# Kernel tuning notes

Measured on AMD Instinct MI355X. Metric: run time of the kernel, lower is better.

Reference implementation:

```python
import jax, jax.numpy as jnp
import numpy as np

N = 4_000_000
H, W = 1080, 1920


def setup_inputs() -> dict:
    key = jax.random.key(0)
    ks = jax.random.split(key, 4)
    # points mostly in front of the camera (viewmat = identity)
    means = jax.random.normal(ks[0], (N, 3), jnp.float32) * jnp.array([2.0, 2.0, 1.5], jnp.float32) + jnp.array([0.0, 0.0, 5.0], jnp.float32)
    colors = jax.random.normal(ks[1], (N, 3), jnp.float32)          # pre-sigmoid logits
    opacities = jax.random.normal(ks[2], (N, 1), jnp.float32)       # pre-sigmoid logits (unused by solid rasterizer)
    scales = jax.random.normal(ks[3], (N, 3), jnp.float32) * 0.1 - 5.0
    quats = jnp.concatenate([jnp.ones((N, 1), jnp.float32), jnp.zeros((N, 3), jnp.float32)], axis=1)
    viewmat = jnp.eye(4, dtype=jnp.float32)
    K = jnp.array([[1000.0, 0.0, W / 2.0], [0.0, 1000.0, H / 2.0], [0.0, 0.0, 1.0]], jnp.float32)
    return dict(means=means, colors=colors, opacities=opacities, scales=scales,
                quats=quats, viewmat=viewmat, K=K, height=H, width=W)


def _rasterize_solid(means, colors, viewmat, K, height, width):
    # camera transform
    R = viewmat[:3, :3]
    t = viewmat[:3, 3]
    mc = means @ R.T + t                     # [N,3] points in camera frame
    z = mc[:, 2]
    front = z > 0.1
    z_safe = jnp.where(front, z, 1.0)        # avoid div-by-~0 for culled points
    fx, fy, cx, cy = K[0, 0], K[1, 1], K[0, 2], K[1, 2]
    x = mc[:, 0] * fx / z_safe + cx
    y = mc[:, 1] * fy / z_safe + cy
    on = front & (x >= 0) & (x < width - 1) & (y >= 0) & (y < height - 1)

    x0f = jnp.floor(x)
    y0f = jnp.floor(y)
    dx = x - x0f
    dy = y - y0f
    x0 = jnp.clip(x0f.astype(jnp.int32), 0, width - 1)
    y0 = jnp.clip(y0f.astype(jnp.int32), 0, height - 1)
    x1 = jnp.clip(x0 + 1, 0, width - 1)
    y1 = jnp.clip(y0 + 1, 0, height - 1)
    pix = y0 * width + x0

    # scatter-min reproduces that order-independently. Off points contribute +inf.
    zbuf = jnp.full((height * width,), jnp.inf, means.dtype).at[pix].min(jnp.where(on, z, jnp.inf))
    zbuf = jax.lax.stop_gradient(zbuf)       # only feeds a boolean test, no grad path in torch either
    vis = on & (z <= zbuf[pix] + 0.05)
    visf = vis.astype(means.dtype)

    # bilinear weights; (wb <-> y1x0, wc <-> y0x1) pairing kept faithful to source
    wa = (1 - dx) * (1 - dy) * visf
    wb = dx * (1 - dy) * visf
    wc = (1 - dx) * dy * visf
    wd = dx * dy * visf

    feat = jnp.concatenate([colors, z[:, None]], axis=1)   # [N,4] rgb+depth
    buf = jnp.zeros((height * width, 5), means.dtype)
    for idx, w in ((pix, wa), (y1 * width + x0, wb), (y0 * width + x1, wc), (y1 * width + x1, wd)):
        buf = buf.at[idx].add(jnp.concatenate([feat * w[:, None], w[:, None]], axis=1))

    total = buf[:, 4:5] + 1e-6
    ff = buf[:, 0:4] / total
    rgb = jnp.clip(ff[:, 0:3], 0.0, 1.0)
    return jnp.concatenate([rgb, ff[:, 3:4]], axis=1).reshape(height, width, 4)


def reference(means, colors, opacities, scales, quats, viewmat, K, height, width):
    render_colors = jax.nn.sigmoid(colors)
    _ = jax.nn.sigmoid(opacities)  # computed in torch forward, unused by solid rasterizer
    return _rasterize_solid(means, render_colors, viewmat, K, height, width)
```

## Files before the change

### kernel.cpp

```cpp
#include <hip/hip_runtime.h>
#include <math.h>

#define IMG_H 1080
#define IMG_W 1920
#define NPIX (IMG_H * IMG_W)

#define TILE_W 64
#define TILE_H 8
#define NTX (IMG_W / TILE_W)
#define NTY (IMG_H / TILE_H)
#define NTILES (NTX * NTY)
#define TPIX (TILE_W * TILE_H)

#define NSEG 512
#define SEGT 1024

#define ZMW (TILE_W + 1)
#define ZMH (TILE_H + 1)
#define NBIN (ZMW * ZMH)

#define CAPT 4096
#define CAP 2048

__device__ __attribute__((noinline)) float4 project4(
    const float* __restrict__ vm, const float* __restrict__ Km,
    float mx, float my, float mz)
{
    float mcx = vm[0] * mx + vm[1] * my + vm[2]  * mz + vm[3];
    float mcy = vm[4] * mx + vm[5] * my + vm[6]  * mz + vm[7];
    float mcz = vm[8] * mx + vm[9] * my + vm[10] * mz + vm[11];
    float z = mcz;
    bool front = z > 0.1f;
    float z_safe = front ? z : 1.0f;
    float x = mcx * Km[0] / z_safe + Km[2];
    float y = mcy * Km[4] / z_safe + Km[5];
    return make_float4(x, y, z, front ? 1.0f : 0.0f);
}

__device__ __forceinline__ bool on_test(const float4& p)
{
    return (p.w != 0.0f) && (p.x >= 0.0f) && (p.x < (float)(IMG_W - 1))
                         && (p.y >= 0.0f) && (p.y < (float)(IMG_H - 1));
}

__device__ __forceinline__ void project_pt(
    const float* __restrict__ vm, const float* __restrict__ Km,
    float mx, float my, float mz,
    float& x, float& y, float& z, bool& on)
{
    float mcx = vm[0] * mx + vm[1] * my + vm[2]  * mz + vm[3];
    float mcy = vm[4] * mx + vm[5] * my + vm[6]  * mz + vm[7];
    float mcz = vm[8] * mx + vm[9] * my + vm[10] * mz + vm[11];
    z = mcz;
    bool front = z > 0.1f;
    float z_safe = front ? z : 1.0f;
    x = mcx * Km[0] / z_safe + Km[2];
    y = mcy * Km[4] / z_safe + Km[5];
    on = front && (x >= 0.0f) && (x < (float)(IMG_W - 1))
               && (y >= 0.0f) && (y < (float)(IMG_H - 1));
}

__global__ __launch_bounds__(SEGT) void k_count(
    const float* __restrict__ means, const float* __restrict__ vm,
    const float* __restrict__ Km, unsigned int* __restrict__ hist,
    int N, int C)
{
    __shared__ unsigned int h[NTILES];
    int tid = threadIdx.x, w = blockIdx.x;
    for (int t = tid; t < NTILES; t += SEGT) h[t] = 0u;
    __syncthreads();
    int start = w * C, end = min(start + C, N);
    for (int j = start + tid; j < end; j += SEGT) {
        float4 p = project4(vm, Km, means[3 * j], means[3 * j + 1], means[3 * j + 2]);
        if (!on_test(p)) continue;
        int x0 = (int)floorf(p.x), y0 = (int)floorf(p.y);
        int tx0 = x0 >> 6, ty0 = y0 >> 3;
        int tx1 = (x0 + 1) >> 6, ty1 = (y0 + 1) >> 3;
#pragma unroll
        for (int sy = 0; sy < 2; ++sy) {
            int ty = sy ? ty1 : ty0;
            if (sy && ty1 == ty0) continue;
#pragma unroll
            for (int sx = 0; sx < 2; ++sx) {
                int tx = sx ? tx1 : tx0;
                if (sx && tx1 == tx0) continue;
                atomicAdd(&h[ty * NTX + tx], 1u);
            }
        }
    }
    __syncthreads();
    for (int t = tid; t < NTILES; t += SEGT)
        hist[(size_t)w * NTILES + t] = h[t];
}

__global__ __launch_bounds__(256) void k_colpref(
    const unsigned int* __restrict__ hist, unsigned int* __restrict__ histBase,
    unsigned int* __restrict__ tileBase)
{
    int t = blockIdx.x * 256 + threadIdx.x;
    if (t >= NTILES) return;
    unsigned int run = 0u;
#pragma unroll 8
    for (int w = 0; w < NSEG; ++w) {
        unsigned int v = hist[(size_t)w * NTILES + t];
        histBase[(size_t)w * NTILES + t] = run;
        run += v;
    }
    tileBase[t] = run;
}

__global__ __launch_bounds__(256) void k_scan(unsigned int* __restrict__ tileBase)
{
    __shared__ unsigned int part[256];
    int tid = threadIdx.x;
    unsigned int loc[16];
    unsigned int sum = 0u;
#pragma unroll
    for (int i = 0; i < 16; ++i) {
        int t = tid * 16 + i;
        unsigned int v = (t < NTILES) ? tileBase[t] : 0u;
        loc[i] = sum;
        sum += v;
    }
    part[tid] = sum;
    __syncthreads();
    if (tid == 0) {
        unsigned int run = 0u;
        for (int i = 0; i < 256; ++i) {
            unsigned int v = part[i];
            part[i] = run;
            run += v;
        }
        tileBase[NTILES] = run;
    }
    __syncthreads();
    unsigned int base = part[tid];
#pragma unroll
    for (int i = 0; i < 16; ++i) {
        int t = tid * 16 + i;
        if (t < NTILES) tileBase[t] = base + loc[i];
    }
}

__global__ __launch_bounds__(SEGT) void k_binscatter(
    const float* __restrict__ means, const float* __restrict__ colors,
    const float* __restrict__ vm, const float* __restrict__ Km,
    const unsigned int* __restrict__ histBase,
    const unsigned int* __restrict__ tileBase,
    float4* __restrict__ records, int N, int C, unsigned int cap)
{
    __shared__ unsigned int cur[NTILES];
    int tid = threadIdx.x, w = blockIdx.x;
    for (int t = tid; t < NTILES; t += SEGT)
        cur[t] = tileBase[t] + histBase[(size_t)w * NTILES + t];
    __syncthreads();
    int start = w * C, end = min(start + C, N);
    for (int j = start + tid; j < end; j += SEGT) {
        float4 p = project4(vm, Km, means[3 * j], means[3 * j + 1], means[3 * j + 2]);
        if (!on_test(p)) continue;
        float r = 1.0f / (1.0f + expf(-colors[3 * j]));
        float g = 1.0f / (1.0f + expf(-colors[3 * j + 1]));
        float b = 1.0f / (1.0f + expf(-colors[3 * j + 2]));
        unsigned int ri = (unsigned int)(r * 1023.0f + 0.5f);
        unsigned int gi = (unsigned int)(g * 1023.0f + 0.5f);
        unsigned int bi = (unsigned int)(b * 1023.0f + 0.5f);
        float4 rec = make_float4(p.x, p.y, p.z,
                                 __uint_as_float(ri | (gi << 10) | (bi << 20)));
        int x0 = (int)floorf(p.x), y0 = (int)floorf(p.y);
        int tx0 = x0 >> 6, ty0 = y0 >> 3;
        int tx1 = (x0 + 1) >> 6, ty1 = (y0 + 1) >> 3;
#pragma unroll
        for (int sy = 0; sy < 2; ++sy) {
            int ty = sy ? ty1 : ty0;
            if (sy && ty1 == ty0) continue;
#pragma unroll
            for (int sx = 0; sx < 2; ++sx) {
                int tx = sx ? tx1 : tx0;
                if (sx && tx1 == tx0) continue;
                int t = ty * NTX + tx;
                unsigned int slot = atomicAdd(&cur[t], 1u);
                if (slot < cap) records[slot] = rec;
            }
        }
    }
}

__global__ __launch_bounds__(256) void k_tile_sort(
    const unsigned int* __restrict__ tileBase,
    const float4* __restrict__ records, float* __restrict__ out,
    unsigned int cap)
{
    __shared__ unsigned short sIdx[CAPT];
    __shared__ int sStart[NBIN + 1];
    __shared__ int sCur[NBIN];
    __shared__ float sZmin[NBIN];
    __shared__ int sScan[256];

    int tid = threadIdx.x;
    int t = blockIdx.x;
    int txb = (t % NTX) * TILE_W;
    int tyb = (t / NTX) * TILE_H;

    unsigned int base = tileBase[t], next = tileBase[t + 1];
    int cnt = 0;
    if (base < cap) cnt = (int)min(min(next - base, cap - base), (unsigned int)CAPT);
    const float4* rec = records + base;

    for (int b = tid; b < NBIN; b += 256) sCur[b] = 0;
    __syncthreads();

    int hb[16];
#pragma unroll
    for (int u = 0; u < 16; ++u) {
        int j = tid + u * 256;
        hb[u] = -1;
        if (j < cnt) {
            float4 v = rec[j];
            int x0l = (int)floorf(v.x) - txb;
            int y0l = (int)floorf(v.y) - tyb;
            int b = (y0l + 1) * ZMW + (x0l + 1);
            hb[u] = b;
            atomicAdd(&sCur[b], 1);
        }
    }
    __syncthreads();

    int b0 = tid * 3;
    int c0 = (b0     < NBIN) ? sCur[b0]     : 0;
    int c1 = (b0 + 1 < NBIN) ? sCur[b0 + 1] : 0;
    int c2 = (b0 + 2 < NBIN) ? sCur[b0 + 2] : 0;
    int local = c0 + c1 + c2;
    sScan[tid] = local;
    __syncthreads();
    for (int off = 1; off < 256; off <<= 1) {
        int v = (tid >= off) ? sScan[tid - off] : 0;
        __syncthreads();
        sScan[tid] += v;
        __syncthreads();
    }
    int run = sScan[tid] - local;
    if (b0 < NBIN)     { sStart[b0]     = run;           sCur[b0]     = run; }
    if (b0 + 1 < NBIN) { sStart[b0 + 1] = run + c0;      sCur[b0 + 1] = run + c0; }
    if (b0 + 2 < NBIN) { sStart[b0 + 2] = run + c0 + c1; sCur[b0 + 2] = run + c0 + c1; }
    if (tid == 255) sStart[NBIN] = cnt;
    __syncthreads();

#pragma unroll
    for (int u = 0; u < 16; ++u) {
        if (hb[u] >= 0) {
            int j = tid + u * 256;
            int slot = atomicAdd(&sCur[hb[u]], 1);
            sIdx[slot] = (unsigned short)j;
        }
    }
    __syncthreads();

    for (int b = tid; b < NBIN; b += 256) {
        float zm = 1e30f;
        int e = sStart[b + 1];
        for (int k = sStart[b]; k < e; ++k)
            zm = fminf(zm, rec[sIdx[k]].z);
        sZmin[b] = zm;
    }
    __syncthreads();

    for (int p = tid; p < TPIX; p += 256) {
        int px = p % TILE_W, py = p / TILE_W;
        float ra = 0.0f, ga = 0.0f, ba = 0.0f, za = 0.0f, wsum = 0.0f;
#pragma unroll
        for (int c = 0; c < 4; ++c) {
            int ox = c & 1, oy = c >> 1;
            int hx = px - ox, hy = py - oy;
            int b = (hy + 1) * ZMW + (hx + 1);
            float zlim = sZmin[b] + 0.05f;
            int e = sStart[b + 1];
            for (int k = sStart[b]; k < e; ++k) {
                float4 v = rec[sIdx[k]];
                if (!(v.z <= zlim)) continue;
                float dx = v.x - floorf(v.x);
                float dy = v.y - floorf(v.y);
                float wgt = (oy ? dx : (1.0f - dx)) * (ox ? dy : (1.0f - dy));
                unsigned int rgb = __float_as_uint(v.w);
                ra += (float)(rgb & 1023u) * wgt;
                ga += (float)((rgb >> 10) & 1023u) * wgt;
                ba += (float)((rgb >> 20) & 1023u) * wgt;
                za += v.z * wgt;
                wsum += wgt;
            }
        }
        float tot = wsum + 1e-6f;
        float inv = (1.0f / 1023.0f) / tot;
        float r = ra * inv, g = ga * inv, b2 = ba * inv;
        float zz = za / tot;
        r  = fminf(fmaxf(r, 0.0f), 1.0f);
        g  = fminf(fmaxf(g, 0.0f), 1.0f);
        b2 = fminf(fmaxf(b2, 0.0f), 1.0f);
        int gy = tyb + py, gx = txb + px;
        reinterpret_cast<float4*>(out)[gy * IMG_W + gx] = make_float4(r, g, b2, zz);
    }
}


__global__ __launch_bounds__(256) void k_zmin(
    const float* __restrict__ means, const float* __restrict__ vm,
    const float* __restrict__ Km, unsigned int* __restrict__ zbuf, int N)
{
    int i = blockIdx.x * 256 + threadIdx.x;
    if (i >= N) return;
    float x, y, z; bool on;
    project_pt(vm, Km, means[3 * i], means[3 * i + 1], means[3 * i + 2], x, y, z, on);
    if (!on) return;
    int x0 = (int)floorf(x), y0 = (int)floorf(y);
    atomicMin(&zbuf[y0 * IMG_W + x0], __float_as_uint(z));
}

__global__ __launch_bounds__(256) void k_scatter_u32(
    const float* __restrict__ means, const float* __restrict__ vm,
    const float* __restrict__ Km, const unsigned int* __restrict__ zbuf,
    unsigned int* __restrict__ cursors, unsigned int* __restrict__ records, int N)
{
    int i = blockIdx.x * 256 + threadIdx.x;
    if (i >= N) return;
    float x, y, z; bool on;
    project_pt(vm, Km, means[3 * i], means[3 * i + 1], means[3 * i + 2], x, y, z, on);
    if (!on) return;
    int x0 = (int)floorf(x), y0 = (int)floorf(y);
    int pix = y0 * IMG_W + x0;
    if (!(z <= __uint_as_float(zbuf[pix]) + 0.05f)) return;
    int tx0 = x0 / TILE_W, ty0 = y0 / TILE_H;
    int tx1 = (x0 + 1) / TILE_W, ty1 = (y0 + 1) / TILE_H;
#pragma unroll
    for (int sy = 0; sy < 2; ++sy) {
        int ty = sy ? ty1 : ty0;
        if (sy && ty1 == ty0) continue;
#pragma unroll
        for (int sx = 0; sx < 2; ++sx) {
            int tx = sx ? tx1 : tx0;
            if (sx && tx1 == tx0) continue;
            int t = ty * NTX + tx;
            unsigned int slot = atomicAdd(&cursors[t], 1u);
            if (slot < CAP) records[(size_t)t * CAP + slot] = (unsigned int)i;
        }
    }
}

__global__ __launch_bounds__(256) void k_tile_u32(
    const float* __restrict__ means, const float* __restrict__ colors,
    const float* __restrict__ vm, const float* __restrict__ Km,
    const unsigned int* __restrict__ cursors,
    const unsigned int* __restrict__ records,
    float* __restrict__ out)
{
    __shared__ float sR[TPIX], sG[TPIX], sB[TPIX], sZ[TPIX], sW[TPIX];
    int tid = threadIdx.x;
    int t = blockIdx.x;
    int txb = (t % NTX) * TILE_W;
    int tyb = (t / NTX) * TILE_H;
    for (int p = tid; p < TPIX; p += 256) {
        sR[p] = 0.0f; sG[p] = 0.0f; sB[p] = 0.0f; sZ[p] = 0.0f; sW[p] = 0.0f;
    }
    __syncthreads();

    int cnt = (int)min(cursors[t], (unsigned int)CAP);
    const unsigned int* rec = records + (size_t)t * CAP;
    for (int j = tid; j < cnt; j += 256) {
        int i = (int)rec[j];
        float x, y, z; bool on;
        project_pt(vm, Km, means[3 * i], means[3 * i + 1], means[3 * i + 2], x, y, z, on);
        float x0f = floorf(x), y0f = floorf(y);
        int x0 = (int)x0f, y0 = (int)y0f;
        float dx = x - x0f, dy = y - y0f;
        float wa = (1.0f - dx) * (1.0f - dy);
        float wb = dx * (1.0f - dy);
        float wc = (1.0f - dx) * dy;
        float wd = dx * dy;
        float r = 1.0f / (1.0f + expf(-colors[3 * i]));
        float g = 1.0f / (1.0f + expf(-colors[3 * i + 1]));
        float b = 1.0f / (1.0f + expf(-colors[3 * i + 2]));
        int cxs[4] = { x0, x0, x0 + 1, x0 + 1 };
        int cys[4] = { y0, y0 + 1, y0, y0 + 1 };
        float ws[4] = { wa, wb, wc, wd };
#pragma unroll
        for (int c = 0; c < 4; ++c) {
            int lx = cxs[c] - txb, ly = cys[c] - tyb;
            if ((unsigned)lx < TILE_W && (unsigned)ly < TILE_H) {
                int lp = ly * TILE_W + lx;
                float w = ws[c];
                atomicAdd(&sR[lp], r * w);
                atomicAdd(&sG[lp], g * w);
                atomicAdd(&sB[lp], b * w);
                atomicAdd(&sZ[lp], z * w);
                atomicAdd(&sW[lp], w);
            }
        }
    }
    __syncthreads();

    for (int p = tid; p < TPIX; p += 256) {
        float tot = sW[p] + 1e-6f;
        float r = sR[p] / tot, g = sG[p] / tot, b = sB[p] / tot, zz = sZ[p] / tot;
        r = fminf(fmaxf(r, 0.0f), 1.0f);
        g = fminf(fmaxf(g, 0.0f), 1.0f);
        b = fminf(fmaxf(b, 0.0f), 1.0f);
        int gy = tyb + p / TILE_W, gx = txb + p % TILE_W;
        reinterpret_cast<float4*>(out)[gy * IMG_W + gx] = make_float4(r, g, b, zz);
    }
}


__global__ __launch_bounds__(256) void k_splat(
    const float* __restrict__ means, const float* __restrict__ colors,
    const float* __restrict__ vm, const float* __restrict__ Km,
    const float* __restrict__ zbuf,
    float* __restrict__ acc, float* __restrict__ wsum, int N)
{
    int i = blockIdx.x * 256 + threadIdx.x;
    if (i >= N) return;
    float x, y, z; bool on;
    project_pt(vm, Km, means[3 * i], means[3 * i + 1], means[3 * i + 2], x, y, z, on);
    if (!on) return;
    float x0f = floorf(x), y0f = floorf(y);
    int x0 = (int)x0f, y0 = (int)y0f;
    int pix = y0 * IMG_W + x0;
    if (!(z <= zbuf[pix] + 0.05f)) return;
    float dx = x - x0f, dy = y - y0f;
    float wa = (1.0f - dx) * (1.0f - dy);
    float wb = dx * (1.0f - dy);
    float wc = (1.0f - dx) * dy;
    float wd = dx * dy;
    float r = 1.0f / (1.0f + expf(-colors[3 * i]));
    float g = 1.0f / (1.0f + expf(-colors[3 * i + 1]));
    float b = 1.0f / (1.0f + expf(-colors[3 * i + 2]));
    int ia = pix, ib = pix + IMG_W, ic = pix + 1, id = pix + IMG_W + 1;
#define SPLAT1(idx, w)                                    \
    do {                                                  \
        atomicAdd(&acc[4 * (idx) + 0], r * (w));          \
        atomicAdd(&acc[4 * (idx) + 1], g * (w));          \
        atomicAdd(&acc[4 * (idx) + 2], b * (w));          \
        atomicAdd(&acc[4 * (idx) + 3], z * (w));          \
        atomicAdd(&wsum[(idx)], (w));                     \
    } while (0)
    SPLAT1(ia, wa); SPLAT1(ib, wb); SPLAT1(ic, wc); SPLAT1(id, wd);
#undef SPLAT1
}

__global__ __launch_bounds__(256) void k_final(
    float* __restrict__ out, const float* __restrict__ wsum)
{
    int p = blockIdx.x * 256 + threadIdx.x;
    if (p >= NPIX) return;
    float tot = wsum[p] + 1e-6f;
    float4 v = reinterpret_cast<float4*>(out)[p];
    float r = v.x / tot, g = v.y / tot, b = v.z / tot, zz = v.w / tot;
    r = fminf(fmaxf(r, 0.0f), 1.0f);
    g = fminf(fmaxf(g, 0.0f), 1.0f);
    b = fminf(fmaxf(b, 0.0f), 1.0f);
    reinterpret_cast<float4*>(out)[p] = make_float4(r, g, b, zz);
}

extern "C" void kernel_launch(void* const* d_in, const int* in_sizes, int n_in,
                              void* d_out, int out_size, void* d_ws, size_t ws_size,
                              hipStream_t stream)
{
    const float* means  = (const float*)d_in[0];
    const float* colors = (const float*)d_in[1];
    const float* vm     = (const float*)d_in[5];
    const float* Km     = (const float*)d_in[6];
    int N = in_sizes[0] / 3;
    float* out = (float*)d_out;

    const size_t histB   = (size_t)NSEG * NTILES * 4;
    const size_t tbB     = (size_t)(NTILES + 1) * 4;
    size_t fixedA        = 2 * histB + tbB;
    fixedA               = (fixedA + 15) & ~(size_t)15;
    const size_t zbufB   = (size_t)NPIX * 4;
    const size_t curB    = (size_t)NTILES * 4;
    const size_t recU32B = (size_t)NTILES * CAP * 4;

    if (ws_size >= fixedA + ((size_t)128 << 20)) {
        unsigned int* hist     = (unsigned int*)d_ws;
        unsigned int* histBase = (unsigned int*)((char*)d_ws + histB);
        unsigned int* tileBase = (unsigned int*)((char*)d_ws + 2 * histB);
        float4*       records  = (float4*)((char*)d_ws + fixedA);
        unsigned int  cap      = (unsigned int)min((ws_size - fixedA) / 16,
                                                   (size_t)0x0FFFFFFF);
        int C = (N + NSEG - 1) / NSEG;
        k_count     <<<NSEG, SEGT, 0, stream>>>(means, vm, Km, hist, N, C);
        k_colpref   <<<(NTILES + 255) / 256, 256, 0, stream>>>(hist, histBase,
                                                               tileBase);
        k_scan      <<<1, 256, 0, stream>>>(tileBase);
        k_binscatter<<<NSEG, SEGT, 0, stream>>>(means, colors, vm, Km,
                                                histBase, tileBase, records,
                                                N, C, cap);
        k_tile_sort <<<NTILES, 256, 0, stream>>>(tileBase, records, out, cap);
    } else if (ws_size >= zbufB + curB + recU32B) {
        unsigned int* zbuf    = (unsigned int*)d_ws;
        unsigned int* cursors = (unsigned int*)((char*)d_ws + zbufB);
        unsigned int* records = (unsigned int*)((char*)d_ws + zbufB + curB);
        int nb = (N + 255) / 256;
        hipMemsetAsync(zbuf, 0x7f, zbufB, stream);
        hipMemsetAsync(cursors, 0, curB, stream);
        k_zmin       <<<nb, 256, 0, stream>>>(means, vm, Km, zbuf, N);
        k_scatter_u32<<<nb, 256, 0, stream>>>(means, vm, Km, zbuf, cursors,
                                              records, N);
        k_tile_u32   <<<NTILES, 256, 0, stream>>>(means, colors, vm, Km,
                                                  cursors, records, out);
    } else {
        unsigned int* zbuf = (unsigned int*)d_ws;
        float*        wsum = (float*)((char*)d_ws + zbufB);
        int nb = (N + 255) / 256;
        hipMemsetAsync(zbuf, 0x7f, zbufB, stream);
        hipMemsetAsync(wsum, 0x00, zbufB, stream);
        hipMemsetAsync(out,  0x00, (size_t)NPIX * 16, stream);
        k_zmin <<<nb, 256, 0, stream>>>(means, vm, Km, zbuf, N);
        k_splat<<<nb, 256, 0, stream>>>(means, colors, vm, Km,
                                        (const float*)zbuf, out, wsum, N);
        k_final<<<(NPIX + 255) / 256, 256, 0, stream>>>(out, wsum);
    }
}
```

Baseline: 419.9 us.

## Split column prefix into chunked scan and stage sorted records in LDS

The per-tile column prefix over 512 segments is split into 8 chunks of 64. A parallel partial-scan kernel writes chunk sums, and a small second scan produces chunk bases that binscatter adds when it initialises its cursors. This raises parallelism beyond the 15 blocks the old single pass launched. The tile kernel now writes bin-sorted float4 records with precomputed fractional offsets into LDS instead of ushort indices, so the z-min and accumulation loops read LDS rather than doing scattered global gathers. In exchange it reads the records from global twice and uses 64KB of LDS per block, which may lower occupancy.

```diff
diff --git a/kernel.cpp b/kernel.cpp
--- a/kernel.cpp
+++ b/kernel.cpp
@@ -14,6 +14,8 @@
 
 #define NSEG 512
 #define SEGT 1024
+#define NCH  (NSEG / 64)
+#define NTB  ((NTILES + 255) / 256)
 
 #define ZMW (TILE_W + 1)
 #define ZMH (TILE_H + 1)
@@ -93,17 +95,37 @@
         hist[(size_t)w * NTILES + t] = h[t];
 }
 
-__global__ __launch_bounds__(256) void k_colpref(
+__global__ __launch_bounds__(256) void k_colpref_part(
     const unsigned int* __restrict__ hist, unsigned int* __restrict__ histBase,
+    unsigned int* __restrict__ chunkSum)
+{
+    int c   = blockIdx.x / NTB;
+    int blk = blockIdx.x % NTB;
+    int t = blk * 256 + threadIdx.x;
+    if (t >= NTILES) return;
+    unsigned int run = 0u;
+    int w0 = c * 64;
+#pragma unroll 8
+    for (int k = 0; k < 64; ++k) {
+        size_t idx = (size_t)(w0 + k) * NTILES + t;
+        unsigned int v = hist[idx];
+        histBase[idx] = run;
+        run += v;
+    }
+    chunkSum[(size_t)c * NTILES + t] = run;
+}
+
+__global__ __launch_bounds__(256) void k_chscan(
+    const unsigned int* __restrict__ chunkSum, unsigned int* __restrict__ chunkBase,
     unsigned int* __restrict__ tileBase)
 {
     int t = blockIdx.x * 256 + threadIdx.x;
     if (t >= NTILES) return;
     unsigned int run = 0u;
-#pragma unroll 8
-    for (int w = 0; w < NSEG; ++w) {
-        unsigned int v = hist[(size_t)w * NTILES + t];
-        histBase[(size_t)w * NTILES + t] = run;
+#pragma unroll
+    for (int c = 0; c < NCH; ++c) {
+        unsigned int v = chunkSum[(size_t)c * NTILES + t];
+        chunkBase[(size_t)c * NTILES + t] = run;
         run += v;
     }
     tileBase[t] = run;
@@ -146,13 +168,16 @@
     const float* __restrict__ means, const float* __restrict__ colors,
     const float* __restrict__ vm, const float* __restrict__ Km,
     const unsigned int* __restrict__ histBase,
+    const unsigned int* __restrict__ chunkBase,
     const unsigned int* __restrict__ tileBase,
     float4* __restrict__ records, int N, int C, unsigned int cap)
 {
     __shared__ unsigned int cur[NTILES];
     int tid = threadIdx.x, w = blockIdx.x;
+    int c = w >> 6;
     for (int t = tid; t < NTILES; t += SEGT)
-        cur[t] = tileBase[t] + histBase[(size_t)w * NTILES + t];
+        cur[t] = tileBase[t] + chunkBase[(size_t)c * NTILES + t]
+                             + histBase[(size_t)w * NTILES + t];
     __syncthreads();
     int start = w * C, end = min(start + C, N);
     for (int j = start + tid; j < end; j += SEGT) {
@@ -185,12 +210,12 @@
     }
 }
 
-__global__ __launch_bounds__(256) void k_tile_sort(
+__global__ __launch_bounds__(256) void k_tile_lds(
     const unsigned int* __restrict__ tileBase,
     const float4* __restrict__ records, float* __restrict__ out,
     unsigned int cap)
 {
-    __shared__ unsigned short sIdx[CAPT];
+    __shared__ float4 sRec[CAPT];
     __shared__ int sStart[NBIN + 1];
     __shared__ int sCur[NBIN];
     __shared__ float sZmin[NBIN];
@@ -209,19 +234,12 @@
     for (int b = tid; b < NBIN; b += 256) sCur[b] = 0;
     __syncthreads();
 
-    int hb[16];
-#pragma unroll
-    for (int u = 0; u < 16; ++u) {
-        int j = tid + u * 256;
-        hb[u] = -1;
-        if (j < cnt) {
-            float4 v = rec[j];
-            int x0l = (int)floorf(v.x) - txb;
-            int y0l = (int)floorf(v.y) - tyb;
-            int b = (y0l + 1) * ZMW + (x0l + 1);
-            hb[u] = b;
-            atomicAdd(&sCur[b], 1);
-        }
+#pragma unroll 4
+    for (int j = tid; j < cnt; j += 256) {
+        float4 v = rec[j];
+        int x0l = (int)floorf(v.x) - txb;
+        int y0l = (int)floorf(v.y) - tyb;
+        atomicAdd(&sCur[(y0l + 1) * ZMW + (x0l + 1)], 1);
     }
     __syncthreads();
 
@@ -245,13 +263,14 @@
     if (tid == 255) sStart[NBIN] = cnt;
     __syncthreads();
 
-#pragma unroll
-    for (int u = 0; u < 16; ++u) {
-        if (hb[u] >= 0) {
-            int j = tid + u * 256;
-            int slot = atomicAdd(&sCur[hb[u]], 1);
-            sIdx[slot] = (unsigned short)j;
-        }
+#pragma unroll 4
+    for (int j = tid; j < cnt; j += 256) {
+        float4 v = rec[j];
+        float x0f = floorf(v.x), y0f = floorf(v.y);
+        int x0l = (int)x0f - txb, y0l = (int)y0f - tyb;
+        int b = (y0l + 1) * ZMW + (x0l + 1);
+        int slot = atomicAdd(&sCur[b], 1);
+        sRec[slot] = make_float4(v.x - x0f, v.y - y0f, v.z, v.w);
     }
     __syncthreads();
 
@@ -259,7 +278,7 @@
         float zm = 1e30f;
         int e = sStart[b + 1];
         for (int k = sStart[b]; k < e; ++k)
-            zm = fminf(zm, rec[sIdx[k]].z);
+            zm = fminf(zm, sRec[k].z);
         sZmin[b] = zm;
     }
     __syncthreads();
@@ -275,10 +294,9 @@
             float zlim = sZmin[b] + 0.05f;
             int e = sStart[b + 1];
             for (int k = sStart[b]; k < e; ++k) {
-                float4 v = rec[sIdx[k]];
+                float4 v = sRec[k];
                 if (!(v.z <= zlim)) continue;
-                float dx = v.x - floorf(v.x);
-                float dy = v.y - floorf(v.y);
+                float dx = v.x, dy = v.y;
                 float wgt = (oy ? dx : (1.0f - dx)) * (ox ? dy : (1.0f - dy));
                 unsigned int rgb = __float_as_uint(v.w);
                 ra += (float)(rgb & 1023u) * wgt;
@@ -470,29 +488,32 @@
     float* out = (float*)d_out;
 
     const size_t histB   = (size_t)NSEG * NTILES * 4;
+    const size_t chB     = (size_t)NCH * NTILES * 4;
     const size_t tbB     = (size_t)(NTILES + 1) * 4;
-    size_t fixedA        = 2 * histB + tbB;
+    size_t fixedA        = 2 * histB + 2 * chB + tbB;
     fixedA               = (fixedA + 15) & ~(size_t)15;
     const size_t zbufB   = (size_t)NPIX * 4;
     const size_t curB    = (size_t)NTILES * 4;
     const size_t recU32B = (size_t)NTILES * CAP * 4;
 
     if (ws_size >= fixedA + ((size_t)128 << 20)) {
-        unsigned int* hist     = (unsigned int*)d_ws;
-        unsigned int* histBase = (unsigned int*)((char*)d_ws + histB);
-        unsigned int* tileBase = (unsigned int*)((char*)d_ws + 2 * histB);
-        float4*       records  = (float4*)((char*)d_ws + fixedA);
-        unsigned int  cap      = (unsigned int)min((ws_size - fixedA) / 16,
-                                                   (size_t)0x0FFFFFFF);
+        unsigned int* hist      = (unsigned int*)d_ws;
+        unsigned int* histBase  = (unsigned int*)((char*)d_ws + histB);
+        unsigned int* chunkSum  = (unsigned int*)((char*)d_ws + 2 * histB);
+        unsigned int* chunkBase = (unsigned int*)((char*)d_ws + 2 * histB + chB);
+        unsigned int* tileBase  = (unsigned int*)((char*)d_ws + 2 * histB + 2 * chB);
+        float4*       records   = (float4*)((char*)d_ws + fixedA);
+        unsigned int  cap       = (unsigned int)min((ws_size - fixedA) / 16,
+                                                    (size_t)0x0FFFFFFF);
         int C = (N + NSEG - 1) / NSEG;
-        k_count     <<<NSEG, SEGT, 0, stream>>>(means, vm, Km, hist, N, C);
-        k_colpref   <<<(NTILES + 255) / 256, 256, 0, stream>>>(hist, histBase,
-                                                               tileBase);
-        k_scan      <<<1, 256, 0, stream>>>(tileBase);
-        k_binscatter<<<NSEG, SEGT, 0, stream>>>(means, colors, vm, Km,
-                                                histBase, tileBase, records,
-                                                N, C, cap);
-        k_tile_sort <<<NTILES, 256, 0, stream>>>(tileBase, records, out, cap);
+        k_count       <<<NSEG, SEGT, 0, stream>>>(means, vm, Km, hist, N, C);
+        k_colpref_part<<<NCH * NTB, 256, 0, stream>>>(hist, histBase, chunkSum);
+        k_chscan      <<<NTB, 256, 0, stream>>>(chunkSum, chunkBase, tileBase);
+        k_scan        <<<1, 256, 0, stream>>>(tileBase);
+        k_binscatter  <<<NSEG, SEGT, 0, stream>>>(means, colors, vm, Km,
+                                                  histBase, chunkBase, tileBase,
+                                                  records, N, C, cap);
+        k_tile_lds    <<<NTILES, 256, 0, stream>>>(tileBase, records, out, cap);
     } else if (ws_size >= zbufB + curB + recU32B) {
         unsigned int* zbuf    = (unsigned int*)d_ws;
         unsigned int* cursors = (unsigned int*)((char*)d_ws + zbufB);
```

Measured after the change: 396.6 us. 5.5% less time.
